# Kernel tuning notes

Measured on AMD Instinct MI355X. Metric: run time of the kernel, lower is better.

Reference implementation:

```python
import jax, jax.numpy as jnp
import numpy as np

N = 10000   # spots (nodes)
E = 60000   # edges (~6 neighbors/spot)
D = 3000    # genes (original_dim)
HID = 128   # intermediate_dim
LAT = 32    # latent_dim
HEADS = 8
NSTATES = 3
MAXIT = 20
KLW = 0.5


def setup_inputs() -> dict:
    key = jax.random.key(0)
    ks = jax.random.split(key, 32)
    s = 0.05
    w = lambda k, shape: (jax.random.normal(k, shape, jnp.float32) * s)
    p = {}
    p['x'] = jax.random.normal(ks[0], (N, D), jnp.float32)
    p['edge_index'] = jax.random.randint(ks[1], (2, E), 0, N, dtype=jnp.int32)
    p['edge_attr'] = jax.random.uniform(ks[2], (E,), jnp.float32)
    # GATConv 1: in=D -> hid, 8 heads (concat=False)
    p['W1'] = w(ks[3], (D, HEADS * HID)); p['a1s'] = w(ks[4], (HEADS, HID)); p['a1d'] = w(ks[5], (HEADS, HID)); p['b1'] = jnp.zeros((HID,), jnp.float32)
    # GATConv 2: hid -> hid, 8 heads
    p['W2'] = w(ks[6], (HID, HEADS * HID)); p['a2s'] = w(ks[7], (HEADS, HID)); p['a2d'] = w(ks[8], (HEADS, HID)); p['b2'] = jnp.zeros((HID,), jnp.float32)
    # GATConv 3: hid -> lat, 1 head
    p['W3'] = w(ks[9], (HID, LAT)); p['a3s'] = w(ks[10], (1, LAT)); p['a3d'] = w(ks[11], (1, LAT)); p['b3'] = jnp.zeros((LAT,), jnp.float32)
    # dense mean / var heads
    p['Wm'] = w(ks[12], (LAT, LAT)); p['bm'] = jnp.zeros((LAT,), jnp.float32)
    p['Wv'] = w(ks[13], (LAT, LAT)); p['bv'] = jnp.zeros((LAT,), jnp.float32)
    # decoder MLP lat -> inter -> D
    p['Wd1'] = w(ks[14], (LAT, HID)); p['bd1'] = jnp.zeros((HID,), jnp.float32)
    p['Wd2'] = w(ks[15], (HID, D)); p['bd2'] = jnp.zeros((D,), jnp.float32)
    return p


def _gat(x, W, a_s, a_d, b, src, dst):
    # PyG GATConv, concat=False (mean over heads), leaky_relu slope 0.2
    H, F = a_s.shape
    h = (x @ W).reshape(N, H, F)                                  # [N,H,F]
    e = jax.nn.leaky_relu(jnp.einsum('nhf,hf->nh', h, a_s)[src]
                          + jnp.einsum('nhf,hf->nh', h, a_d)[dst], 0.2)  # [E',H]
    emax = jax.ops.segment_max(e, dst, num_segments=N)
    ee = jnp.exp(e - emax[dst])
    den = jax.ops.segment_sum(ee, dst, num_segments=N)
    alpha = ee / (den[dst] + 1e-16)
    out = jax.ops.segment_sum(alpha[:, :, None] * h[src], dst, num_segments=N)
    return out.mean(axis=1) + b


def _forward(x, edge_attr, W1, a1s, a1d, b1, W2, a2s, a2d, b2, W3, a3s, a3d, b3,
             Wm, bm, Wv, bv, Wd1, bd1, Wd2, bd2, edge_index):
    loops = jnp.arange(N, dtype=edge_index.dtype)  # GATConv adds self-loops
    src = jnp.concatenate([edge_index[0], loops])
    dst = jnp.concatenate([edge_index[1], loops])
    h = jax.nn.relu(_gat(x, W1, a1s, a1d, b1, src, dst))
    h = jax.nn.relu(_gat(h, W2, a2s, a2d, b2, src, dst))
    z = _gat(h, W3, a3s, a3d, b3, src, dst)
    z_mean = z @ Wm + bm
    z_var = jnp.clip(jnp.exp(z @ Wv + bv), 1e-8, 100.0)
    recon = jax.nn.relu(z @ Wd1 + bd1) @ Wd2 + bd2                 # [N,D]

    # ---- CNEncoder: vectorized Metropolis-Hastings over all spots ----
    sm = jax.lax.stop_gradient(recon.mean(axis=1, keepdims=True))  # detached in torch
    sm = (sm - sm.mean()) / (sm.std() + 1e-8)                      # [N,1]
    m = jax.lax.stop_gradient(recon.mean(axis=1))
    # likelihood(state) sums exp(-0.5*(spot_mean - mean[state])^2); state in 0..2
    L = jnp.sum(jnp.exp(-0.5 * (sm - m[:NSTATES][None, :]) ** 2), axis=0)  # [3]
    prior = jnp.array([0.1, 0.8, 0.1], jnp.float32)
    trans = jnp.array([[0.98, 0.01, 0.01], [0.01, 0.98, 0.01], [0.01, 0.01, 0.98]], jnp.float32)
    # acceptance ratio[cand, cur] = prior ratio * likelihood ratio * transition ratio
    ratio = (prior[:, None] / prior[None, :]) * (L[:, None] / L[None, :]) * (trans.T / trans)

    kmc = jax.random.key(42)
    k0, kscan = jax.random.split(kmc)
    states0 = jax.random.randint(k0, (N,), 0, NSTATES)
    probs0 = jnp.zeros((N, NSTATES), jnp.float32)

    def step(carry, k):
        states, probs = carry
        k1, k2 = jax.random.split(k)
        cand = jax.random.randint(k1, (N,), 0, NSTATES)
        u = jax.random.uniform(k2, (N,))
        states = jnp.where(u < ratio[cand, states], cand, states)
        return (states, probs + jax.nn.one_hot(states, NSTATES, dtype=probs.dtype)), None

    (_, probs), _ = jax.lax.scan(step, (states0, probs0), jax.random.split(kscan, MAXIT))

    # scatter_mean of state_probs[row] onto col
    row, col = edge_index[0], edge_index[1]
    sums = jax.ops.segment_sum(probs[row], col, num_segments=N)
    cnt = jax.ops.segment_sum(jnp.ones((E,), jnp.float32), col, num_segments=N)
    smoothed = sums / jnp.maximum(cnt, 1.0)[:, None]
    st = (jnp.argmax(smoothed, axis=1) + 1).astype(jnp.float32)[:, None]  # [N,1]

    sac = recon * st
    nc = sac / (sac.sum(axis=1, keepdims=True) + 1e-8) * x.sum(axis=1, keepdims=True)
    rmin = jax.lax.stop_gradient(nc.min()) * 0.8   # .item() in torch -> constant
    rmax = jax.lax.stop_gradient(nc.max()) * 1.2
    nc = (nc - nc.min()) / (nc.max() - nc.min() + 1e-8)
    nc = nc * (rmax - rmin) + rmin
    nc = nc / nc.mean()
    reg_loss = jnp.sum(recon ** 2) * 1e-4

    kl_loss = jnp.sum(-0.5 * jnp.log(z_var) + 0.5 * (z_var + z_mean ** 2) - 0.5, axis=1) * KLW
    return nc, recon, kl_loss, reg_loss


def reference(x, edge_index, edge_attr, W1, a1s, a1d, b1, W2, a2s, a2d, b2,
              W3, a3s, a3d, b3, Wm, bm, Wv, bv, Wd1, bd1, Wd2, bd2):
    return _forward(x, edge_attr, W1, a1s, a1d, b1, W2, a2s, a2d, b2,
                    W3, a3s, a3d, b3, Wm, bm, Wv, bv, Wd1, bd1, Wd2, bd2, edge_index)
```

## Files before the change

kernel.cpp:

```cpp
#include <hip/hip_runtime.h>
#include <cstdint>
#include <cstddef>

#define N_NODES 10000
#define DIM     3000
#define NEDGE   60000
#define EPLUS   (NEDGE + N_NODES)
#define HIDF    128
#define LATF    32
#define NHEAD   8
#define MAXDEG  256
#define NCBLK   2048
static const size_t TOTAL_NC = (size_t)N_NODES * DIM;

typedef short bf16x8 __attribute__((ext_vector_type(8)));
typedef float f32x4  __attribute__((ext_vector_type(4)));

__device__ __forceinline__ ushort bf16rn(float f) {
  unsigned u = __float_as_uint(f);
  return (ushort)((u + 0x7FFFu + ((u >> 16) & 1u)) >> 16);
}
__device__ __forceinline__ float bf16f(ushort h) {
  return __uint_as_float((unsigned)h << 16);
}

__global__ void k_count(const int* __restrict__ ei, int* __restrict__ cnt) {
  int e = blockIdx.x * blockDim.x + threadIdx.x;
  if (e >= EPLUS) return;
  int dst = (e < NEDGE) ? ei[NEDGE + e] : (e - NEDGE);
  atomicAdd(&cnt[dst], 1);
}

__global__ void k_scan(const int* __restrict__ cnt, int* __restrict__ rowptr) {
  constexpr int ITEMS = (N_NODES + 1023) / 1024;
  __shared__ int s[1024];
  int t = threadIdx.x;
  int base = t * ITEMS;
  int loc[ITEMS];
  int sum = 0;
  for (int i = 0; i < ITEMS; i++) {
    int idx = base + i;
    int v = (idx < N_NODES) ? cnt[idx] : 0;
    loc[i] = sum;
    sum += v;
  }
  s[t] = sum;
  __syncthreads();
  for (int off = 1; off < 1024; off <<= 1) {
    int v = 0;
    if (t >= off) v = s[t - off];
    __syncthreads();
    if (t >= off) s[t] += v;
    __syncthreads();
  }
  int prefix = (t == 0) ? 0 : s[t - 1];
  for (int i = 0; i < ITEMS; i++) {
    int idx = base + i;
    if (idx < N_NODES) rowptr[idx] = prefix + loc[i];
  }
  if (t == 1023) rowptr[N_NODES] = prefix + sum;
}

__global__ void k_fill(const int* __restrict__ ei, const int* __restrict__ rowptr,
                       int* __restrict__ fill, int* __restrict__ esrc) {
  int e = blockIdx.x * blockDim.x + threadIdx.x;
  if (e >= EPLUS) return;
  int src, dst;
  if (e < NEDGE) { src = ei[e]; dst = ei[NEDGE + e]; }
  else           { src = e - NEDGE; dst = e - NEDGE; }
  int pos = atomicAdd(&fill[dst], 1);
  esrc[rowptr[dst] + pos] = src;
}

__global__ void k_split3(const float* __restrict__ src, ushort* __restrict__ ph,
                         ushort* __restrict__ pm, ushort* __restrict__ pl, size_t n4)
{
  size_t stride = (size_t)gridDim.x * blockDim.x;
  for (size_t i = (size_t)blockIdx.x * blockDim.x + threadIdx.x; i < n4; i += stride) {
    float4 v = ((const float4*)src)[i];
    float f[4] = {v.x, v.y, v.z, v.w};
    ushort hh[4], mm[4], ll[4];
#pragma unroll
    for (int j = 0; j < 4; j++) {
      ushort h = bf16rn(f[j]);
      float r1 = f[j] - bf16f(h);
      ushort m = bf16rn(r1);
      float r2 = r1 - bf16f(m);
      ushort l = bf16rn(r2);
      hh[j] = h; mm[j] = m; ll[j] = l;
    }
    ((ushort4*)ph)[i] = make_ushort4(hh[0], hh[1], hh[2], hh[3]);
    ((ushort4*)pm)[i] = make_ushort4(mm[0], mm[1], mm[2], mm[3]);
    ((ushort4*)pl)[i] = make_ushort4(ll[0], ll[1], ll[2], ll[3]);
  }
}

__global__ void k_tsplit3(const float* __restrict__ W, ushort* __restrict__ Th,
                          ushort* __restrict__ Tm, ushort* __restrict__ Tl,
                          int K, int Nc, int Ks)
{
  __shared__ float tile[32][33];
  int tx = threadIdx.x & 31, ty = threadIdx.x >> 5;
  int n0 = blockIdx.x * 32, k0 = blockIdx.y * 32;
#pragma unroll
  for (int i = 0; i < 4; i++) {
    int k = k0 + ty + i * 8, n = n0 + tx;
    tile[ty + i * 8][tx] = (k < K && n < Nc) ? W[(size_t)k * Nc + n] : 0.f;
  }
  __syncthreads();
#pragma unroll
  for (int i = 0; i < 4; i++) {
    int n = n0 + ty + i * 8, k = k0 + tx;
    if (n < Nc && k < Ks) {
      float v = tile[tx][ty + i * 8];
      ushort h = bf16rn(v);
      float r1 = v - bf16f(h);
      ushort m = bf16rn(r1);
      float r2 = r1 - bf16f(m);
      ushort l = bf16rn(r2);
      size_t o = (size_t)n * Ks + k;
      Th[o] = h; Tm[o] = m; Tl[o] = l;
    }
  }
}

__device__ __forceinline__ void gld_lds16(const ushort* g, ushort* l) {
  __builtin_amdgcn_global_load_lds(
      (const __attribute__((address_space(1))) void*)g,
      (__attribute__((address_space(3))) void*)l,
      16, 0, 0);
}

__global__ __launch_bounds__(256, 3) void gemm_split3(
    const ushort* __restrict__ Ah, const ushort* __restrict__ Am, const ushort* __restrict__ Al, int lda,
    const ushort* __restrict__ Bh, const ushort* __restrict__ Bm, const ushort* __restrict__ Bl, int ldb,
    const float* __restrict__ bias, float* __restrict__ C,
    int M, int Nc, int ksteps, int relu)
{
  __shared__ ushort As[3][128][32];
  __shared__ ushort Bs[3][128][32];
  int t = threadIdx.x;

  int nwg = gridDim.x * gridDim.y;
  int bid = blockIdx.y * gridDim.x + blockIdx.x;
  int cpx = nwg >> 3;
  int w   = (bid & 7) * cpx + (bid >> 3);
  int bn  = (w % gridDim.x) * 128;
  int bm  = (w / gridDim.x) * 128;

  int wave = t >> 6, lane = t & 63;
  int wm = (wave >> 1) * 64, wn = (wave & 1) * 64;
  int q = lane >> 4, l15 = lane & 15;

  size_t offA[2], offB[2];
  int lofs[2];
#pragma unroll
  for (int i = 0; i < 2; i++) {
    int c = i * 256 + t;
    int r = c >> 2, cc = c & 3;
    int ccg = cc ^ ((r >> 1) & 3);
    int ga = bm + r; if (ga > M - 1) ga = M - 1;
    int gb = bn + r; if (gb > Nc - 1) gb = Nc - 1;
    offA[i] = (size_t)ga * lda + (size_t)(ccg * 8);
    offB[i] = (size_t)gb * ldb + (size_t)(ccg * 8);
    lofs[i] = c * 8;
  }
  int fs = (q ^ ((l15 >> 1) & 3)) * 8;

  f32x4 acc[4][4];
#pragma unroll
  for (int i = 0; i < 4; i++)
#pragma unroll
    for (int j = 0; j < 4; j++) acc[i][j] = (f32x4){0.f, 0.f, 0.f, 0.f};

  for (int ks = 0; ks < ksteps; ks++) {
    int k0 = ks * 32;
#pragma unroll
    for (int i = 0; i < 2; i++) {
      gld_lds16(Ah + offA[i] + k0, &As[0][0][0] + lofs[i]);
      gld_lds16(Am + offA[i] + k0, &As[1][0][0] + lofs[i]);
      gld_lds16(Al + offA[i] + k0, &As[2][0][0] + lofs[i]);
      gld_lds16(Bh + offB[i] + k0, &Bs[0][0][0] + lofs[i]);
      gld_lds16(Bm + offB[i] + k0, &Bs[1][0][0] + lofs[i]);
      gld_lds16(Bl + offB[i] + k0, &Bs[2][0][0] + lofs[i]);
    }
    __syncthreads();
    bf16x8 bh[4], bmv[4], bl[4];
#pragma unroll
    for (int j = 0; j < 4; j++) {
      bh[j]  = *(const bf16x8*)&Bs[0][wn + j * 16 + l15][fs];
      bmv[j] = *(const bf16x8*)&Bs[1][wn + j * 16 + l15][fs];
      bl[j]  = *(const bf16x8*)&Bs[2][wn + j * 16 + l15][fs];
    }
#pragma unroll
    for (int i = 0; i < 4; i++) {
      bf16x8 ah = *(const bf16x8*)&As[0][wm + i * 16 + l15][fs];
      bf16x8 am = *(const bf16x8*)&As[1][wm + i * 16 + l15][fs];
      bf16x8 al = *(const bf16x8*)&As[2][wm + i * 16 + l15][fs];
#pragma unroll
      for (int j = 0; j < 4; j++) {
        acc[i][j] = __builtin_amdgcn_mfma_f32_16x16x32_bf16(ah, bh[j],  acc[i][j], 0, 0, 0);
        acc[i][j] = __builtin_amdgcn_mfma_f32_16x16x32_bf16(ah, bmv[j], acc[i][j], 0, 0, 0);
        acc[i][j] = __builtin_amdgcn_mfma_f32_16x16x32_bf16(am, bh[j],  acc[i][j], 0, 0, 0);
        acc[i][j] = __builtin_amdgcn_mfma_f32_16x16x32_bf16(am, bmv[j], acc[i][j], 0, 0, 0);
        acc[i][j] = __builtin_amdgcn_mfma_f32_16x16x32_bf16(ah, bl[j],  acc[i][j], 0, 0, 0);
        acc[i][j] = __builtin_amdgcn_mfma_f32_16x16x32_bf16(al, bh[j],  acc[i][j], 0, 0, 0);
      }
    }
    __syncthreads();
  }
#pragma unroll
  for (int i = 0; i < 4; i++) {
#pragma unroll
    for (int r = 0; r < 4; r++) {
      int row = bm + wm + i * 16 + q * 4 + r;
      if (row >= M) continue;
#pragma unroll
      for (int j = 0; j < 4; j++) {
        int col = bn + wn + j * 16 + l15;
        if (col >= Nc) continue;
        float v = acc[i][j][r] + (bias ? bias[col] : 0.f);
        if (relu) v = fmaxf(v, 0.f);
        C[(size_t)row * Nc + col] = v;
      }
    }
  }
}

#define BM 64
#define BN 64
#define BK 16
__global__ __launch_bounds__(256) void gemm_f32(
    const float* __restrict__ A, const float* __restrict__ B,
    const float* __restrict__ bias, float* __restrict__ C,
    int M, int Nc, int K, int relu)
{
  __shared__ float As[BK][BM + 4];
  __shared__ float Bs[BK][BN + 4];
  int bm = blockIdx.y * BM, bn = blockIdx.x * BN;
  int t = threadIdx.x;
  int tm = (t / 16) * 4;
  int tn = (t % 16) * 4;
  float acc[4][4] = {};
  for (int k0 = 0; k0 < K; k0 += BK) {
    for (int i = t; i < BK * BM; i += 256) {
      int kk = i % BK, mm = i / BK;
      int gm = bm + mm, gk = k0 + kk;
      As[kk][mm] = (gm < M && gk < K) ? A[(size_t)gm * K + gk] : 0.f;
    }
    for (int i = t; i < BK * BN; i += 256) {
      int kk = i / BN, nn = i % BN;
      int gk = k0 + kk, gn = bn + nn;
      Bs[kk][nn] = (gk < K && gn < Nc) ? B[(size_t)gk * Nc + gn] : 0.f;
    }
    __syncthreads();
#pragma unroll
    for (int kk = 0; kk < BK; kk++) {
      float a[4], b[4];
#pragma unroll
      for (int i = 0; i < 4; i++) a[i] = As[kk][tm + i];
#pragma unroll
      for (int j = 0; j < 4; j++) b[j] = Bs[kk][tn + j];
#pragma unroll
      for (int i = 0; i < 4; i++)
#pragma unroll
        for (int j = 0; j < 4; j++) acc[i][j] += a[i] * b[j];
    }
    __syncthreads();
  }
  for (int i = 0; i < 4; i++) {
    int gm = bm + tm + i;
    if (gm >= M) continue;
    for (int j = 0; j < 4; j++) {
      int gn = bn + tn + j;
      if (gn >= Nc) continue;
      float v = acc[i][j] + (bias ? bias[gn] : 0.f);
      if (relu) v = fmaxf(v, 0.f);
      C[(size_t)gm * Nc + gn] = v;
    }
  }
}

__global__ void k_attdot(const float* __restrict__ hbuf, const float* __restrict__ a_s,
                         const float* __restrict__ a_d, float* __restrict__ as_,
                         float* __restrict__ ad_, int H, int F, int total)
{
  int wid = blockIdx.x * 4 + (threadIdx.x >> 6);
  int lane = threadIdx.x & 63;
  if (wid >= total) return;
  int h = wid % H;
  float s1 = 0.f, s2 = 0.f;
  const float* hr = hbuf + (size_t)wid * F;
  for (int f = lane; f < F; f += 64) {
    float hv = hr[f];
    s1 += hv * a_s[h * F + f];
    s2 += hv * a_d[h * F + f];
  }
  for (int off = 32; off > 0; off >>= 1) {
    s1 += __shfl_down(s1, off);
    s2 += __shfl_down(s2, off);
  }
  if (lane == 0) { as_[wid] = s1; ad_[wid] = s2; }
}

__global__ __launch_bounds__(256) void k_gat_agg8(
    const float* __restrict__ hbuf, const float* __restrict__ as_,
    const float* __restrict__ ad_, const float* __restrict__ bias,
    const int* __restrict__ rowptr, const int* __restrict__ esrc,
    float* __restrict__ out, int relu)
{
  const int H = 8, F = 128;
  int n = blockIdx.x;
  int t = threadIdx.x;
  __shared__ float s_a[MAXDEG][8];
  __shared__ int   s_src[MAXDEG];
  __shared__ float s_out[2][128];
  int beg = rowptr[n];
  int deg = rowptr[n + 1] - beg;
  if (deg > MAXDEG) deg = MAXDEG;
  for (int j = t; j < deg; j += 256) s_src[j] = esrc[beg + j];
  __syncthreads();
  for (int idx = t; idx < deg * H; idx += 256) {
    int j = idx >> 3, h = idx & 7;
    float v = as_[(size_t)s_src[j] * H + h] + ad_[(size_t)n * H + h];
    s_a[j][h] = (v > 0.f) ? v : 0.2f * v;
  }
  __syncthreads();
  if (t < H) {
    float m = -3.4e38f;
    for (int j = 0; j < deg; j++) m = fmaxf(m, s_a[j][t]);
    float den = 0.f;
    for (int j = 0; j < deg; j++) { float e = expf(s_a[j][t] - m); s_a[j][t] = e; den += e; }
    float inv = 1.0f / (den + 1e-16f);
    for (int j = 0; j < deg; j++) s_a[j][t] *= inv;
  }
  __syncthreads();
  int f = t & 127;
  int hg = t >> 7;
  float acc = 0.f;
  for (int h = hg; h < H; h += 2)
    for (int j = 0; j < deg; j++)
      acc += s_a[j][h] * hbuf[(size_t)s_src[j] * (H * F) + h * F + f];
  s_out[hg][f] = acc;
  __syncthreads();
  if (hg == 0) {
    float v = (s_out[0][f] + s_out[1][f]) * 0.125f + bias[f];
    if (relu) v = fmaxf(v, 0.f);
    out[(size_t)n * F + f] = v;
  }
}

__global__ void k_gat_agg1(const float* __restrict__ hbuf, const float* __restrict__ as_,
                           const float* __restrict__ ad_, const float* __restrict__ bias,
                           const int* __restrict__ rowptr, const int* __restrict__ esrc,
                           float* __restrict__ out)
{
  int n = blockIdx.x, t = threadIdx.x;
  __shared__ float s_a[MAXDEG];
  __shared__ int   s_src[MAXDEG];
  int beg = rowptr[n];
  int deg = rowptr[n + 1] - beg;
  if (deg > MAXDEG) deg = MAXDEG;
  for (int j = t; j < deg; j += 64) {
    int s = s_src[j] = esrc[beg + j];
    float v = as_[s] + ad_[n];
    s_a[j] = (v > 0.f) ? v : 0.2f * v;
  }
  __syncthreads();
  if (t == 0) {
    float m = -3.4e38f;
    for (int j = 0; j < deg; j++) m = fmaxf(m, s_a[j]);
    float den = 0.f;
    for (int j = 0; j < deg; j++) { float e = expf(s_a[j] - m); s_a[j] = e; den += e; }
    float inv = 1.0f / (den + 1e-16f);
    for (int j = 0; j < deg; j++) s_a[j] *= inv;
  }
  __syncthreads();
  if (t < 32) {
    float acc = 0.f;
    for (int j = 0; j < deg; j++) acc += s_a[j] * hbuf[(size_t)s_src[j] * 32 + t];
    out[(size_t)n * 32 + t] = acc + bias[t];
  }
}

__global__ void k_kl(const float* __restrict__ z, const float* __restrict__ Wm,
                     const float* __restrict__ bm, const float* __restrict__ Wv,
                     const float* __restrict__ bv, float* __restrict__ kl)
{
  int n = blockIdx.x * 8 + (threadIdx.x >> 5);
  int l = threadIdx.x & 31;
  if (n >= N_NODES) return;
  float zm = bm[l], zv = bv[l];
  const float* zr = z + (size_t)n * LATF;
  for (int k = 0; k < LATF; k++) {
    float zk = zr[k];
    zm += zk * Wm[k * LATF + l];
    zv += zk * Wv[k * LATF + l];
  }
  float var = expf(zv);
  var = fminf(fmaxf(var, 1e-8f), 100.0f);
  float term = -0.5f * logf(var) + 0.5f * (var + zm * zm) - 0.5f;
  for (int off = 16; off > 0; off >>= 1) term += __shfl_down(term, off, 32);
  if (l == 0) kl[n] = term * 0.5f;
}

__global__ void k_rowstats(const float* __restrict__ recon, const float* __restrict__ x,
                           float* __restrict__ rsum, float* __restrict__ xsum,
                           float* __restrict__ regp)
{
  int n = blockIdx.x, t = threadIdx.x;
  const float* rr = recon + (size_t)n * DIM;
  const float* xr = x + (size_t)n * DIM;
  float s1 = 0.f, s2 = 0.f, sq = 0.f;
  for (int d = t; d < DIM; d += 256) {
    float r = rr[d];
    s1 += r; sq += r * r;
    s2 += xr[d];
  }
  __shared__ float sh[3][256];
  sh[0][t] = s1; sh[1][t] = s2; sh[2][t] = sq;
  __syncthreads();
  for (int off = 128; off > 0; off >>= 1) {
    if (t < off) {
      sh[0][t] += sh[0][t + off];
      sh[1][t] += sh[1][t + off];
      sh[2][t] += sh[2][t + off];
    }
    __syncthreads();
  }
  if (t == 0) { rsum[n] = sh[0][0]; xsum[n] = sh[1][0]; regp[n] = sh[2][0]; }
}

__global__ void k_reduce_reg(const float* __restrict__ regp, float* __restrict__ out_reg) {
  __shared__ double s[256];
  int t = threadIdx.x;
  double acc = 0.0;
  for (int i = t; i < N_NODES; i += 256) acc += (double)regp[i];
  s[t] = acc;
  __syncthreads();
  for (int off = 128; off > 0; off >>= 1) { if (t < off) s[t] += s[t + off]; __syncthreads(); }
  if (t == 0) out_reg[0] = (float)(s[0] * 1e-4);
}

__global__ void k_ncraw(const float* __restrict__ recon, const float* __restrict__ rsum,
                        const float* __restrict__ xsum, float* __restrict__ ncraw,
                        float* __restrict__ pmin, float* __restrict__ pmax,
                        float* __restrict__ psum)
{
  int t = threadIdx.x;
  float lmin = 3.4e38f, lmax = -3.4e38f, lsum = 0.f;
  size_t stride = (size_t)gridDim.x * 256;
  for (size_t i = (size_t)blockIdx.x * 256 + t; i < TOTAL_NC; i += stride) {
    int n = (int)(i / DIM);
    float v = recon[i] / (rsum[n] + 1e-8f) * xsum[n];
    ncraw[i] = v;
    lmin = fminf(lmin, v); lmax = fmaxf(lmax, v); lsum += v;
  }
  __shared__ float smin[256], smax[256], ssum[256];
  smin[t] = lmin; smax[t] = lmax; ssum[t] = lsum;
  __syncthreads();
  for (int off = 128; off > 0; off >>= 1) {
    if (t < off) {
      smin[t] = fminf(smin[t], smin[t + off]);
      smax[t] = fmaxf(smax[t], smax[t + off]);
      ssum[t] += ssum[t + off];
    }
    __syncthreads();
  }
  if (t == 0) { pmin[blockIdx.x] = smin[0]; pmax[blockIdx.x] = smax[0]; psum[blockIdx.x] = ssum[0]; }
}

__global__ void k_consts(const float* __restrict__ pmin, const float* __restrict__ pmax,
                         const float* __restrict__ psum, float* __restrict__ consts)
{
  __shared__ float smin[256], smax[256];
  __shared__ double ssum[256];
  int t = threadIdx.x;
  float lmin = 3.4e38f, lmax = -3.4e38f;
  double ls = 0.0;
  for (int i = t; i < NCBLK; i += 256) {
    lmin = fminf(lmin, pmin[i]); lmax = fmaxf(lmax, pmax[i]); ls += (double)psum[i];
  }
  smin[t] = lmin; smax[t] = lmax; ssum[t] = ls;
  __syncthreads();
  for (int off = 128; off > 0; off >>= 1) {
    if (t < off) {
      smin[t] = fminf(smin[t], smin[t + off]);
      smax[t] = fmaxf(smax[t], smax[t + off]);
      ssum[t] += ssum[t + off];
    }
    __syncthreads();
  }
  if (t == 0) {
    float gmin = smin[0], gmax = smax[0];
    float meanv = (float)(ssum[0] / (double)TOTAL_NC);
    float rmin = gmin * 0.8f, rmax = gmax * 1.2f;
    float aa = (rmax - rmin) / (gmax - gmin + 1e-8f);
    float bb = rmin - aa * gmin;
    float meant = aa * meanv + bb;
    consts[0] = aa; consts[1] = bb; consts[2] = 1.0f / meant;
  }
}

__global__ void k_scale(float* __restrict__ nc, const float* __restrict__ consts) {
  float aa = consts[0], bb = consts[1], invm = consts[2];
  size_t stride = (size_t)gridDim.x * 256;
  for (size_t i = (size_t)blockIdx.x * 256 + threadIdx.x; i < TOTAL_NC; i += stride) {
    nc[i] = (aa * nc[i] + bb) * invm;
  }
}

extern "C" void kernel_launch(void* const* d_in, const int* in_sizes, int n_in,
                              void* d_out, int out_size, void* d_ws, size_t ws_size,
                              hipStream_t stream)
{
  const float* x   = (const float*)d_in[0];
  const int*   ei  = (const int*)d_in[1];
  const float* W1  = (const float*)d_in[3];
  const float* a1s = (const float*)d_in[4];
  const float* a1d = (const float*)d_in[5];
  const float* b1  = (const float*)d_in[6];
  const float* W2  = (const float*)d_in[7];
  const float* a2s = (const float*)d_in[8];
  const float* a2d = (const float*)d_in[9];
  const float* b2  = (const float*)d_in[10];
  const float* W3  = (const float*)d_in[11];
  const float* a3s = (const float*)d_in[12];
  const float* a3d = (const float*)d_in[13];
  const float* b3  = (const float*)d_in[14];
  const float* Wm  = (const float*)d_in[15];
  const float* bm  = (const float*)d_in[16];
  const float* Wv  = (const float*)d_in[17];
  const float* bv  = (const float*)d_in[18];
  const float* Wd1 = (const float*)d_in[19];
  const float* bd1 = (const float*)d_in[20];
  const float* Wd2 = (const float*)d_in[21];
  const float* bd2 = (const float*)d_in[22];

  float* out_nc    = (float*)d_out;
  float* out_recon = out_nc + 30000000;
  float* out_kl    = out_nc + 60000000;
  float* out_reg   = out_nc + 60010000;

  ushort* xh   = (ushort*)out_recon;
  ushort* xm   = (ushort*)(out_recon + 15000000);
  ushort* xl   = (ushort*)out_nc;
  float*  h1buf = out_nc + 15000000;
  ushort* W1h  = (ushort*)(out_nc + 25250000);
  ushort* W1m  = (ushort*)(out_nc + 26800000);
  ushort* W1l  = (ushort*)(out_nc + 28350000);
  ushort* bBh  = (ushort*)(out_nc + 0);
  ushort* bBm  = (ushort*)(out_nc + 700000);
  ushort* bBl  = (ushort*)(out_nc + 1400000);
  ushort* hdh  = (ushort*)(out_nc + 2100000);
  ushort* hdm  = (ushort*)(out_nc + 2800000);
  ushort* hdl  = (ushort*)(out_nc + 3500000);
  ushort* Wd2h = (ushort*)(out_nc + 4500000);
  ushort* Wd2m = (ushort*)(out_nc + 4700000);
  ushort* Wd2l = (ushort*)(out_nc + 4900000);
  ushort* W2h  = (ushort*)(out_nc + 5200000);
  ushort* W2m  = (ushort*)(out_nc + 5300000);
  ushort* W2l  = (ushort*)(out_nc + 5400000);

  float* wsf    = (float*)d_ws;
  float* bufB   = wsf + 0;
  float* bufC   = wsf + 1300000;
  float* hd     = wsf + 2600000;
  float* as_    = wsf + 3900000;
  float* ad_    = wsf + 4000000;
  float* zbuf   = wsf + 4100000;
  float* h3h    = wsf + 4450000;
  float* rsum   = wsf + 4800000;
  float* xsum   = wsf + 4820000;
  float* regp   = wsf + 4840000;
  float* pminb  = wsf + 4860000;
  float* pmaxb  = wsf + 4880000;
  float* psumb  = wsf + 4900000;
  float* consts = wsf + 4920000;
  int* rowptr = (int*)(wsf + 5000000);
  int* cntb   = rowptr + 10016;
  int* esrc   = cntb + 10016;

  k_split3<<<4096, 256, 0, stream>>>(x, xh, xm, xl, 30000000 / 4);
  k_tsplit3<<<dim3(32, 94), 256, 0, stream>>>(W1, W1h, W1m, W1l, 3000, 1024, 3008);
  hipMemsetAsync(cntb, 0, N_NODES * sizeof(int), stream);
  k_count<<<(EPLUS + 255) / 256, 256, 0, stream>>>(ei, cntb);
  k_scan<<<1, 1024, 0, stream>>>(cntb, rowptr);
  hipMemsetAsync(cntb, 0, N_NODES * sizeof(int), stream);
  k_fill<<<(EPLUS + 255) / 256, 256, 0, stream>>>(ei, rowptr, cntb, esrc);

  gemm_split3<<<dim3(8, 79), 256, 0, stream>>>(xh, xm, xl, 3000, W1h, W1m, W1l, 3008,
                                               nullptr, h1buf, N_NODES, 1024, 94, 0);
  k_attdot<<<(N_NODES * NHEAD + 3) / 4, 256, 0, stream>>>(h1buf, a1s, a1d, as_, ad_, NHEAD, HIDF, N_NODES * NHEAD);
  k_gat_agg8<<<N_NODES, 256, 0, stream>>>(h1buf, as_, ad_, b1, rowptr, esrc, bufB, 1);

  k_tsplit3<<<dim3(32, 4), 256, 0, stream>>>(W2, W2h, W2m, W2l, 128, 1024, 128);
  k_split3<<<512, 256, 0, stream>>>(bufB, bBh, bBm, bBl, 1280000 / 4);
  gemm_split3<<<dim3(8, 79), 256, 0, stream>>>(bBh, bBm, bBl, 128, W2h, W2m, W2l, 128,
                                               nullptr, h1buf, N_NODES, 1024, 4, 0);
  k_attdot<<<(N_NODES * NHEAD + 3) / 4, 256, 0, stream>>>(h1buf, a2s, a2d, as_, ad_, NHEAD, HIDF, N_NODES * NHEAD);
  k_gat_agg8<<<N_NODES, 256, 0, stream>>>(h1buf, as_, ad_, b2, rowptr, esrc, bufC, 1);

  gemm_f32<<<dim3(1, (N_NODES + BM - 1) / BM), 256, 0, stream>>>(bufC, W3, nullptr, h3h, N_NODES, LATF, HIDF, 0);
  k_attdot<<<(N_NODES + 3) / 4, 256, 0, stream>>>(h3h, a3s, a3d, as_, ad_, 1, LATF, N_NODES);
  k_gat_agg1<<<N_NODES, 64, 0, stream>>>(h3h, as_, ad_, b3, rowptr, esrc, zbuf);

  k_kl<<<(N_NODES + 7) / 8, 256, 0, stream>>>(zbuf, Wm, bm, Wv, bv, out_kl);

  gemm_f32<<<dim3(2, (N_NODES + BM - 1) / BM), 256, 0, stream>>>(zbuf, Wd1, bd1, hd, N_NODES, HIDF, LATF, 1);
  k_split3<<<512, 256, 0, stream>>>(hd, hdh, hdm, hdl, 1280000 / 4);
  k_tsplit3<<<dim3(94, 4), 256, 0, stream>>>(Wd2, Wd2h, Wd2m, Wd2l, 128, 3000, 128);
  gemm_split3<<<dim3(24, 79), 256, 0, stream>>>(hdh, hdm, hdl, 128, Wd2h, Wd2m, Wd2l, 128,
                                                bd2, out_recon, N_NODES, DIM, 4, 0);

  k_rowstats<<<N_NODES, 256, 0, stream>>>(out_recon, x, rsum, xsum, regp);
  k_reduce_reg<<<1, 256, 0, stream>>>(regp, out_reg);
  k_ncraw<<<NCBLK, 256, 0, stream>>>(out_recon, rsum, xsum, out_nc, pminb, pmaxb, psumb);
  k_consts<<<1, 256, 0, stream>>>(pminb, pmaxb, psumb, consts);
  k_scale<<<4096, 256, 0, stream>>>(out_nc, consts);

  (void)in_sizes; (void)n_in; (void)out_size; (void)ws_size;
}
```

Baseline: 1.271 ms.

## Double-buffer LDS tiles in split-bf16 GEMM to overlap loads with MFMA

Turns the split-3 bf16 GEMM's shared-memory tiles into two buffers. The next K-slice is prefetched via global_load_lds while the current slice feeds the MFMAs, and one of the two barriers per step is dropped. This doubles LDS to 48KB per block and changes the launch-bounds occupancy hint from 3 to 1. Because the loads go straight to LDS, the wait at the single end-of-loop barrier may not cover the async copies, so correctness depends on the compiler inserting vmcnt waits.

```diff
diff --git a/kernel.cpp b/kernel.cpp
--- a/kernel.cpp
+++ b/kernel.cpp
@@ -131,14 +131,14 @@
       16, 0, 0);
 }
 
-__global__ __launch_bounds__(256, 3) void gemm_split3(
+__global__ __launch_bounds__(256, 1) void gemm_split3(
     const ushort* __restrict__ Ah, const ushort* __restrict__ Am, const ushort* __restrict__ Al, int lda,
     const ushort* __restrict__ Bh, const ushort* __restrict__ Bm, const ushort* __restrict__ Bl, int ldb,
     const float* __restrict__ bias, float* __restrict__ C,
     int M, int Nc, int ksteps, int relu)
 {
-  __shared__ ushort As[3][128][32];
-  __shared__ ushort Bs[3][128][32];
+  __shared__ ushort As[2][3][128][32];
+  __shared__ ushort Bs[2][3][128][32];
   int t = threadIdx.x;
 
   int nwg = gridDim.x * gridDim.y;
@@ -167,36 +167,43 @@
   }
   int fs = (q ^ ((l15 >> 1) & 3)) * 8;
 
+  auto stage = [&](int buf, int k0) {
+#pragma unroll
+    for (int i = 0; i < 2; i++) {
+      gld_lds16(Ah + offA[i] + k0, &As[buf][0][0][0] + lofs[i]);
+      gld_lds16(Am + offA[i] + k0, &As[buf][1][0][0] + lofs[i]);
+      gld_lds16(Al + offA[i] + k0, &As[buf][2][0][0] + lofs[i]);
+      gld_lds16(Bh + offB[i] + k0, &Bs[buf][0][0][0] + lofs[i]);
+      gld_lds16(Bm + offB[i] + k0, &Bs[buf][1][0][0] + lofs[i]);
+      gld_lds16(Bl + offB[i] + k0, &Bs[buf][2][0][0] + lofs[i]);
+    }
+  };
+
   f32x4 acc[4][4];
 #pragma unroll
   for (int i = 0; i < 4; i++)
 #pragma unroll
     for (int j = 0; j < 4; j++) acc[i][j] = (f32x4){0.f, 0.f, 0.f, 0.f};
 
+  stage(0, 0);
+  __syncthreads();
+
   for (int ks = 0; ks < ksteps; ks++) {
-    int k0 = ks * 32;
-#pragma unroll
-    for (int i = 0; i < 2; i++) {
-      gld_lds16(Ah + offA[i] + k0, &As[0][0][0] + lofs[i]);
-      gld_lds16(Am + offA[i] + k0, &As[1][0][0] + lofs[i]);
-      gld_lds16(Al + offA[i] + k0, &As[2][0][0] + lofs[i]);
-      gld_lds16(Bh + offB[i] + k0, &Bs[0][0][0] + lofs[i]);
-      gld_lds16(Bm + offB[i] + k0, &Bs[1][0][0] + lofs[i]);
-      gld_lds16(Bl + offB[i] + k0, &Bs[2][0][0] + lofs[i]);
-    }
-    __syncthreads();
+    int cur = ks & 1;
+    if (ks + 1 < ksteps) stage(cur ^ 1, (ks + 1) * 32);
+
     bf16x8 bh[4], bmv[4], bl[4];
 #pragma unroll
     for (int j = 0; j < 4; j++) {
-      bh[j]  = *(const bf16x8*)&Bs[0][wn + j * 16 + l15][fs];
-      bmv[j] = *(const bf16x8*)&Bs[1][wn + j * 16 + l15][fs];
-      bl[j]  = *(const bf16x8*)&Bs[2][wn + j * 16 + l15][fs];
+      bh[j]  = *(const bf16x8*)&Bs[cur][0][wn + j * 16 + l15][fs];
+      bmv[j] = *(const bf16x8*)&Bs[cur][1][wn + j * 16 + l15][fs];
+      bl[j]  = *(const bf16x8*)&Bs[cur][2][wn + j * 16 + l15][fs];
     }
 #pragma unroll
     for (int i = 0; i < 4; i++) {
-      bf16x8 ah = *(const bf16x8*)&As[0][wm + i * 16 + l15][fs];
-      bf16x8 am = *(const bf16x8*)&As[1][wm + i * 16 + l15][fs];
-      bf16x8 al = *(const bf16x8*)&As[2][wm + i * 16 + l15][fs];
+      bf16x8 ah = *(const bf16x8*)&As[cur][0][wm + i * 16 + l15][fs];
+      bf16x8 am = *(const bf16x8*)&As[cur][1][wm + i * 16 + l15][fs];
+      bf16x8 al = *(const bf16x8*)&As[cur][2][wm + i * 16 + l15][fs];
 #pragma unroll
       for (int j = 0; j < 4; j++) {
         acc[i][j] = __builtin_amdgcn_mfma_f32_16x16x32_bf16(ah, bh[j],  acc[i][j], 0, 0, 0);
@@ -209,6 +216,7 @@
     }
     __syncthreads();
   }
+
 #pragma unroll
   for (int i = 0; i < 4; i++) {
 #pragma unroll
```

Result: slower. 1.624 ms (+27.7%).
